# Kernel optimization log

Hardware: AMD Instinct MI355X
Metric: run time of the kernel (lower is better)

Reference implementation:

```python
import jax, jax.numpy as jnp
import numpy as np

EPS = 1e-8


def _mp_match(v1, v2, w):
    """Fused multi-perspective cosine match.
    v1, v2: (G, L, D); w: (P, D). Returns (G, L, P).
    cos_p(l) = <w_p*v1_l, w_p*v2_l> / max(||w_p*v1_l|| * ||w_p*v2_l||, eps)
    """
    w2 = w * w  # (P, D)
    num = jnp.einsum('gld,pd->glp', v1 * v2, w2)
    n1 = jnp.sqrt(jnp.einsum('gld,pd->glp', v1 * v1, w2))
    n2 = jnp.sqrt(jnp.einsum('gld,pd->glp', v2 * v2, w2))
    return num / jnp.maximum(n1 * n2, EPS)


def setup_inputs() -> dict:
    key = jax.random.key(0)
    k1, k2 = jax.random.split(key)
    n_graphs = 64
    nodes_per_graph = 2048
    dim = 128  # must equal perspectives (mp_w is square)
    N = n_graphs * nodes_per_graph
    feats = jax.random.normal(k1, (N, dim), dtype=jnp.float32)
    graph_idx = jnp.repeat(jnp.arange(n_graphs, dtype=jnp.int64), nodes_per_graph)
    mp_w = jax.random.uniform(k2, (dim, dim), dtype=jnp.float32)  # torch.rand
    return {"feats": feats, "mp_w": mp_w, "graph_idx": graph_idx, "n_graphs": n_graphs}


def reference(feats, mp_w, graph_idx, n_graphs):
    N, d = feats.shape
    L = N // n_graphs  # equal-size graphs, graph_idx is sorted/contiguous
    g = feats.reshape(n_graphs, L, d)
    p = g[0::2]  # (G/2, L, d) premise graphs
    h = g[1::2]  # (G/2, L, d) hypothesis graphs
    # cosine_attention is a plain dot product (no normalization in source)
    att = jnp.einsum('gld,gmd->glm', p, h)        # (G/2, Lp, Lh)
    att_p = jnp.einsum('glm,gmd->gld', att, h)     # (G/2, Lp, d)
    att_h = jnp.einsum('glm,gld->gmd', att, p)     # (G/2, Lh, d)
    multi_p = _mp_match(p, att_p, mp_w)            # (G/2, Lp, P)
    multi_h = _mp_match(h, att_h, mp_w)            # (G/2, Lh, P)
    # original concatenates [p0, h0, p1, h1, ...] along node axis
    P = mp_w.shape[0]
    out = jnp.stack([multi_p, multi_h], axis=1).reshape(n_graphs * L, P)
    return out
```

## Files before the change

kernel.cpp:

```cpp
#include <hip/hip_runtime.h>
#include <math.h>

#define D 128
#define GRAPHS 64

typedef __attribute__((ext_vector_type(8))) short bf16x8;
typedef __attribute__((ext_vector_type(4))) float f32x4;

union U4H8 { uint4 u; bf16x8 h; };

__device__ __forceinline__ unsigned short f2bf(float f) {
  union { float f; unsigned u; } v; v.f = f;
  unsigned r = v.u + 0x7fffu + ((v.u >> 16) & 1u);
  return (unsigned short)(r >> 16);
}
__device__ __forceinline__ unsigned asu(float f) {
  union { float f; unsigned u; } v; v.f = f; return v.u;
}
__device__ __forceinline__ float asf(unsigned u) {
  union { unsigned u; float f; } v; v.u = u; return v.f;
}

__device__ __forceinline__ int swzA(int u) {
  return u ^ (((((u >> 8) ^ (u >> 4)) & 3) ^ ((u >> 3) & 1)) << 1);
}
__device__ __forceinline__ int swzB(int u) {
  return u ^ ((((u >> 9) ^ (u >> 4)) & 3) << 1);
}

__global__ __launch_bounds__(256, 2) void gram_partial_kernel(
    const float* __restrict__ feats, unsigned short* __restrict__ partial,
    int L, int KS) {
  const int g = blockIdx.x / KS;
  const int sl = blockIdx.x - g * KS;
  const int chunk = L / KS;
  const float* __restrict__ X = feats + ((size_t)g * L + (size_t)sl * chunk) * D;

  __shared__ __align__(16) unsigned short smem[16384];
  const int tid = threadIdx.x;
  const int wv = tid >> 6, lane = tid & 63, quad = lane >> 4, ln = lane & 15;

  f32x4 acc[2][8];
#pragma unroll
  for (int rt = 0; rt < 2; ++rt)
#pragma unroll
    for (int ct = 0; ct < 8; ++ct) acc[rt][ct] = (f32x4)(0.f);

  int k2v[4], d4v[4];
#pragma unroll
  for (int v = 0; v < 4; ++v) {
    int tt = tid + v * 256;
    k2v[v] = tt & 31;
    d4v[v] = tt >> 5;
  }
  float4 pf[8];
#pragma unroll
  for (int v = 0; v < 4; ++v) {
    pf[2 * v] = *(const float4*)(X + (size_t)(2 * k2v[v]) * D + 4 * d4v[v]);
    pf[2 * v + 1] = *(const float4*)(X + (size_t)(2 * k2v[v] + 1) * D + 4 * d4v[v]);
  }

  for (int it = 0; it < chunk; it += 64) {
    __syncthreads();
#pragma unroll
    for (int v = 0; v < 4; ++v) {
      const float* p0 = (const float*)&pf[2 * v];
      const float* p1 = (const float*)&pf[2 * v + 1];
      int k = 2 * k2v[v];
      int ks = k >> 5, kk = k & 31, qs = kk >> 3, j = kk & 7;
#pragma unroll
      for (int i = 0; i < 4; ++i) {
        int d = 4 * d4v[v] + i, t = d >> 4, lnw = d & 15;
        *(unsigned*)&smem[((ks * 8 + t) * 64 + qs * 16 + lnw) * 8 + j] =
            (unsigned)f2bf(p0[i]) | ((unsigned)f2bf(p1[i]) << 16);
      }
    }
    __syncthreads();
    if (it + 64 < chunk) {
      const float* Xn = X + (size_t)(it + 64) * D;
#pragma unroll
      for (int v = 0; v < 4; ++v) {
        pf[2 * v] = *(const float4*)(Xn + (size_t)(2 * k2v[v]) * D + 4 * d4v[v]);
        pf[2 * v + 1] =
            *(const float4*)(Xn + (size_t)(2 * k2v[v] + 1) * D + 4 * d4v[v]);
      }
    }
#pragma unroll
    for (int ks = 0; ks < 2; ++ks) {
      bf16x8 af[2], bfr[8];
      af[0] = *(const bf16x8*)&smem[((ks * 8 + 2 * wv) * 64 + lane) * 8];
      af[1] = *(const bf16x8*)&smem[((ks * 8 + 2 * wv + 1) * 64 + lane) * 8];
#pragma unroll
      for (int ct = 0; ct < 8; ++ct)
        bfr[ct] = *(const bf16x8*)&smem[((ks * 8 + ct) * 64 + lane) * 8];
#pragma unroll
      for (int rt = 0; rt < 2; ++rt)
#pragma unroll
        for (int ct = 0; ct < 8; ++ct)
          acc[rt][ct] = __builtin_amdgcn_mfma_f32_16x16x32_bf16(
              af[rt], bfr[ct], acc[rt][ct], 0, 0, 0);
    }
  }

  __syncthreads();
#pragma unroll
  for (int rt = 0; rt < 2; ++rt)
#pragma unroll
    for (int ct = 0; ct < 8; ++ct)
#pragma unroll
      for (int r = 0; r < 4; ++r)
        smem[(32 * wv + 16 * rt + quad * 4 + r) * 128 + 16 * ct + ln] =
            f2bf(acc[rt][ct][r]);
  __syncthreads();
  unsigned short* P = partial + ((size_t)sl * GRAPHS + g) * (D * D);
#pragma unroll
  for (int v = 0; v < 8; ++v) {
    int idx = tid + v * 256;
    *(uint4*)&P[(size_t)idx * 8] = *(uint4*)&smem[idx * 8];
  }
}

__global__ __launch_bounds__(256) void reduce_w2_kernel(
    const unsigned short* __restrict__ partial, unsigned short* __restrict__ gram,
    const float* __restrict__ w, unsigned short* __restrict__ w2, int KS) {
  const int bid = blockIdx.x;
  if (bid < 512) {
    int idx = bid * 256 + threadIdx.x;
    int e8 = idx * 8;
    int g = e8 >> 14, e = e8 & (D * D - 1);
    float s[8];
#pragma unroll
    for (int i = 0; i < 8; ++i) s[i] = 0.f;
    for (int sl = 0; sl < KS; ++sl) {
      uint4 t = *(const uint4*)&partial[((size_t)sl * GRAPHS + g) * (D * D) + e];
      const unsigned* tp = &t.x;
#pragma unroll
      for (int q = 0; q < 4; ++q) {
        s[2 * q] += asf(tp[q] << 16);
        s[2 * q + 1] += asf(tp[q] & 0xFFFF0000u);
      }
    }
    uint4 o;
    o.x = (unsigned)f2bf(s[0]) | ((unsigned)f2bf(s[1]) << 16);
    o.y = (unsigned)f2bf(s[2]) | ((unsigned)f2bf(s[3]) << 16);
    o.z = (unsigned)f2bf(s[4]) | ((unsigned)f2bf(s[5]) << 16);
    o.w = (unsigned)f2bf(s[6]) | ((unsigned)f2bf(s[7]) << 16);
    *(uint4*)&gram[(size_t)g * (D * D) + e] = o;
  } else {
    int idx = (bid - 512) * 256 + threadIdx.x;
    const float* src = w + (size_t)idx * 8;
    float4 a = *(const float4*)src;
    float4 b = *(const float4*)(src + 4);
    uint4 o;
    o.x = (unsigned)f2bf(a.x * a.x) | ((unsigned)f2bf(a.y * a.y) << 16);
    o.y = (unsigned)f2bf(a.z * a.z) | ((unsigned)f2bf(a.w * a.w) << 16);
    o.z = (unsigned)f2bf(b.x * b.x) | ((unsigned)f2bf(b.y * b.y) << 16);
    o.w = (unsigned)f2bf(b.z * b.z) | ((unsigned)f2bf(b.w * b.w) << 16);
    *(uint4*)&w2[(size_t)idx * 8] = o;
  }
}

__global__ __launch_bounds__(512, 4) void fused_kernel4(
    const float* __restrict__ feats, const unsigned short* __restrict__ gram,
    const unsigned short* __restrict__ w2, float* __restrict__ out, int L) {
  const int tiles = L >> 6;
  const int gi = blockIdx.x / tiles;
  const int row0 = (blockIdx.x - gi * tiles) << 6;
  const float* __restrict__ A = feats + ((size_t)gi * L + row0) * D;
  const unsigned short* __restrict__ G = gram + (size_t)(gi ^ 1) * (D * D);
  float* __restrict__ O = out + ((size_t)gi * L + row0) * D;

  __shared__ __align__(16) unsigned short sAf[8192];
  __shared__ __align__(16) unsigned short sVf[8192];
  __shared__ __align__(16) unsigned short sBf[16384];

  const int tid = threadIdx.x;
  const int wv = tid >> 6, lane = tid & 63, quad = lane >> 4, ln = lane & 15;
  const int rowg = wv >> 1, colg = wv & 1;

#pragma unroll
  for (int v = 0; v < 4; ++v) {
    int idx = tid + v * 512;
    int r = idx >> 5, c4 = idx & 31;
    float4 t = *(const float4*)(A + (size_t)r * D + c4 * 4);
    int kc = c4 >> 3, qd = (c4 & 7) >> 1, j0 = (c4 & 1) * 4;
    int rt = r >> 4, lnw = r & 15;
    uint2 pk;
    pk.x = (unsigned)f2bf(t.x) | ((unsigned)f2bf(t.y) << 16);
    pk.y = (unsigned)f2bf(t.z) | ((unsigned)f2bf(t.w) << 16);
    *(uint2*)&sAf[swzA((kc * 4 + rt) * 64 + qd * 16 + lnw) * 8 + j0] = pk;
  }
#pragma unroll
  for (int v = 0; v < 4; ++v) {
    int idx = tid + v * 512;
    int r = idx >> 4, c16 = idx & 15;
    uint4 t = *(const uint4*)(G + (size_t)r * D + c16 * 8);
    int kc = c16 >> 2, qd = c16 & 3, tb = r >> 4, lnw = r & 15;
    *(uint4*)&sBf[swzB((kc * 8 + tb) * 64 + qd * 16 + lnw) * 8] = t;
  }
  __syncthreads();

  f32x4 acc1[4];
#pragma unroll
  for (int c = 0; c < 4; ++c) acc1[c] = (f32x4)(0.f);
#pragma unroll
  for (int kc = 0; kc < 4; ++kc) {
    bf16x8 af = *(const bf16x8*)&sAf[swzA((kc * 4 + rowg) * 64 + lane) * 8];
#pragma unroll
    for (int c = 0; c < 4; ++c) {
      int ct = colg * 4 + c;
      bf16x8 bfr = *(const bf16x8*)&sBf[swzB((kc * 8 + ct) * 64 + lane) * 8];
      acc1[c] = __builtin_amdgcn_mfma_f32_16x16x32_bf16(af, bfr, acc1[c], 0, 0, 0);
    }
  }
#pragma unroll
  for (int c = 0; c < 4; ++c)
#pragma unroll
    for (int r = 0; r < 4; ++r) {
      int col = (colg * 4 + c) * 16 + ln;
      int kc_t = col >> 5, q_t = (col >> 3) & 3, j_t = col & 7;
      sVf[swzA((kc_t * 4 + rowg) * 64 + q_t * 16 + quad * 4 + r) * 8 + j_t] =
          f2bf(acc1[c][r]);
    }
  __syncthreads();

#pragma unroll
  for (int v = 0; v < 4; ++v) {
    int idx = tid + v * 512;
    int r = idx >> 4, c16 = idx & 15;
    uint4 t = *(const uint4*)(w2 + (size_t)r * D + c16 * 8);
    int kc = c16 >> 2, qd = c16 & 3, tb = r >> 4, lnw = r & 15;
    *(uint4*)&sBf[swzB((kc * 8 + tb) * 64 + qd * 16 + lnw) * 8] = t;
  }
  __syncthreads();

  f32x4 an[4], s1[4], s2[4];
#pragma unroll
  for (int c = 0; c < 4; ++c) {
    an[c] = (f32x4)(0.f);
    s1[c] = (f32x4)(0.f);
    s2[c] = (f32x4)(0.f);
  }
#pragma unroll
  for (int dc = 0; dc < 4; ++dc) {
    uint4 ua = *(const uint4*)&sAf[swzA((dc * 4 + rowg) * 64 + lane) * 8];
    uint4 uv = *(const uint4*)&sVf[swzA((dc * 4 + rowg) * 64 + lane) * 8];
    U4H8 fx2, faa, fvv;
    const unsigned* uap = &ua.x;
    const unsigned* uvp = &uv.x;
#pragma unroll
    for (int q = 0; q < 4; ++q) {
      float a0 = asf(uap[q] << 16), a1 = asf(uap[q] & 0xFFFF0000u);
      float v0 = asf(uvp[q] << 16), v1 = asf(uvp[q] & 0xFFFF0000u);
      (&fx2.u.x)[q] = __builtin_amdgcn_perm(asu(a1 * v1), asu(a0 * v0), 0x07060302u);
      (&faa.u.x)[q] = __builtin_amdgcn_perm(asu(a1 * a1), asu(a0 * a0), 0x07060302u);
      (&fvv.u.x)[q] = __builtin_amdgcn_perm(asu(v1 * v1), asu(v0 * v0), 0x07060302u);
    }
#pragma unroll
    for (int c = 0; c < 4; ++c) {
      int ct = colg * 4 + c;
      bf16x8 wf = *(const bf16x8*)&sBf[swzB((dc * 8 + ct) * 64 + lane) * 8];
      an[c] = __builtin_amdgcn_mfma_f32_16x16x32_bf16(fx2.h, wf, an[c], 0, 0, 0);
      s1[c] = __builtin_amdgcn_mfma_f32_16x16x32_bf16(faa.h, wf, s1[c], 0, 0, 0);
      s2[c] = __builtin_amdgcn_mfma_f32_16x16x32_bf16(fvv.h, wf, s2[c], 0, 0, 0);
    }
  }

#pragma unroll
  for (int c = 0; c < 4; ++c)
#pragma unroll
    for (int r = 0; r < 4; ++r) {
      float t = fmaxf(s1[c][r] * s2[c][r], 1e-16f);
      O[(size_t)(rowg * 16 + quad * 4 + r) * D + (colg * 4 + c) * 16 + ln] =
          an[c][r] * __builtin_amdgcn_rsqf(t);
    }
}

extern "C" void kernel_launch(void* const* d_in, const int* in_sizes, int n_in,
                              void* d_out, int out_size, void* d_ws, size_t ws_size,
                              hipStream_t stream) {
  const float* feats = (const float*)d_in[0];
  const float* w = (const float*)d_in[1];
  float* out = (float*)d_out;
  const int L = (in_sizes[0] / D) / GRAPHS;

  const size_t partSlice = (size_t)GRAPHS * D * D * sizeof(unsigned short);
  const size_t gramB = partSlice;
  const size_t w2B = (size_t)D * D * sizeof(unsigned short);
  int KS = 16;
  while (KS > 1 && (size_t)KS * partSlice + gramB + w2B > ws_size) KS >>= 1;

  unsigned short* partialBuf = (unsigned short*)d_ws;
  unsigned short* gramBuf = partialBuf + (size_t)KS * GRAPHS * D * D;
  unsigned short* w2Buf = gramBuf + (size_t)GRAPHS * D * D;

  hipLaunchKernelGGL(gram_partial_kernel, dim3(GRAPHS * KS), dim3(256), 0,
                     stream, feats, partialBuf, L, KS);
  hipLaunchKernelGGL(reduce_w2_kernel, dim3(520), dim3(256), 0, stream,
                     partialBuf, gramBuf, w, w2Buf, KS);
  hipLaunchKernelGGL(fused_kernel4, dim3(GRAPHS * (L >> 6)), dim3(512), 0,
                     stream, feats, gramBuf, w2Buf, out, L);
}
```

Measured before the change: 157.0 us.

## Reuse A tile smem for attention output and split epilogue to raise occupancy

Drops the separate sVf shared buffer. The attention-weighted tile is written back into the sAf buffer after a barrier, and the original A fragments are kept in registers. The final multi-perspective MFMA stage is split into two passes over column pairs to cut accumulator register pressure, and launch bounds are raised to 6 blocks per CU. The goal is higher occupancy for this latency-bound fused kernel, at the cost of extra register-held fragments and recomputing the elementwise products per pass.

```diff
diff --git a/kernel.cpp b/kernel.cpp
--- a/kernel.cpp
+++ b/kernel.cpp
@@ -160,7 +160,7 @@
   }
 }
 
-__global__ __launch_bounds__(512, 4) void fused_kernel4(
+__global__ __launch_bounds__(512, 6) void fused_kernel4(
     const float* __restrict__ feats, const unsigned short* __restrict__ gram,
     const unsigned short* __restrict__ w2, float* __restrict__ out, int L) {
   const int tiles = L >> 6;
@@ -171,7 +171,6 @@
   float* __restrict__ O = out + ((size_t)gi * L + row0) * D;
 
   __shared__ __align__(16) unsigned short sAf[8192];
-  __shared__ __align__(16) unsigned short sVf[8192];
   __shared__ __align__(16) unsigned short sBf[16384];
 
   const int tid = threadIdx.x;
@@ -200,30 +199,32 @@
   }
   __syncthreads();
 
+  U4H8 uaf[4];
   f32x4 acc1[4];
 #pragma unroll
   for (int c = 0; c < 4; ++c) acc1[c] = (f32x4)(0.f);
 #pragma unroll
   for (int kc = 0; kc < 4; ++kc) {
-    bf16x8 af = *(const bf16x8*)&sAf[swzA((kc * 4 + rowg) * 64 + lane) * 8];
+    uaf[kc].u = *(const uint4*)&sAf[swzA((kc * 4 + rowg) * 64 + lane) * 8];
 #pragma unroll
     for (int c = 0; c < 4; ++c) {
       int ct = colg * 4 + c;
       bf16x8 bfr = *(const bf16x8*)&sBf[swzB((kc * 8 + ct) * 64 + lane) * 8];
-      acc1[c] = __builtin_amdgcn_mfma_f32_16x16x32_bf16(af, bfr, acc1[c], 0, 0, 0);
-    }
-  }
+      acc1[c] = __builtin_amdgcn_mfma_f32_16x16x32_bf16(uaf[kc].h, bfr,
+                                                        acc1[c], 0, 0, 0);
+    }
+  }
+  __syncthreads();
+
 #pragma unroll
   for (int c = 0; c < 4; ++c)
 #pragma unroll
     for (int r = 0; r < 4; ++r) {
       int col = (colg * 4 + c) * 16 + ln;
       int kc_t = col >> 5, q_t = (col >> 3) & 3, j_t = col & 7;
-      sVf[swzA((kc_t * 4 + rowg) * 64 + q_t * 16 + quad * 4 + r) * 8 + j_t] =
+      sAf[swzA((kc_t * 4 + rowg) * 64 + q_t * 16 + quad * 4 + r) * 8 + j_t] =
           f2bf(acc1[c][r]);
     }
-  __syncthreads();
-
 #pragma unroll
   for (int v = 0; v < 4; ++v) {
     int idx = tid + v * 512;
@@ -234,46 +235,52 @@
   }
   __syncthreads();
 
-  f32x4 an[4], s1[4], s2[4];
-#pragma unroll
-  for (int c = 0; c < 4; ++c) {
-    an[c] = (f32x4)(0.f);
-    s1[c] = (f32x4)(0.f);
-    s2[c] = (f32x4)(0.f);
-  }
-#pragma unroll
-  for (int dc = 0; dc < 4; ++dc) {
-    uint4 ua = *(const uint4*)&sAf[swzA((dc * 4 + rowg) * 64 + lane) * 8];
-    uint4 uv = *(const uint4*)&sVf[swzA((dc * 4 + rowg) * 64 + lane) * 8];
-    U4H8 fx2, faa, fvv;
-    const unsigned* uap = &ua.x;
-    const unsigned* uvp = &uv.x;
-#pragma unroll
-    for (int q = 0; q < 4; ++q) {
-      float a0 = asf(uap[q] << 16), a1 = asf(uap[q] & 0xFFFF0000u);
-      float v0 = asf(uvp[q] << 16), v1 = asf(uvp[q] & 0xFFFF0000u);
-      (&fx2.u.x)[q] = __builtin_amdgcn_perm(asu(a1 * v1), asu(a0 * v0), 0x07060302u);
-      (&faa.u.x)[q] = __builtin_amdgcn_perm(asu(a1 * a1), asu(a0 * a0), 0x07060302u);
-      (&fvv.u.x)[q] = __builtin_amdgcn_perm(asu(v1 * v1), asu(v0 * v0), 0x07060302u);
-    }
-#pragma unroll
-    for (int c = 0; c < 4; ++c) {
-      int ct = colg * 4 + c;
-      bf16x8 wf = *(const bf16x8*)&sBf[swzB((dc * 8 + ct) * 64 + lane) * 8];
-      an[c] = __builtin_amdgcn_mfma_f32_16x16x32_bf16(fx2.h, wf, an[c], 0, 0, 0);
-      s1[c] = __builtin_amdgcn_mfma_f32_16x16x32_bf16(faa.h, wf, s1[c], 0, 0, 0);
-      s2[c] = __builtin_amdgcn_mfma_f32_16x16x32_bf16(fvv.h, wf, s2[c], 0, 0, 0);
-    }
-  }
-
-#pragma unroll
-  for (int c = 0; c < 4; ++c)
-#pragma unroll
-    for (int r = 0; r < 4; ++r) {
-      float t = fmaxf(s1[c][r] * s2[c][r], 1e-16f);
-      O[(size_t)(rowg * 16 + quad * 4 + r) * D + (colg * 4 + c) * 16 + ln] =
-          an[c][r] * __builtin_amdgcn_rsqf(t);
-    }
+#pragma unroll
+  for (int cp = 0; cp < 2; ++cp) {
+    f32x4 an[2], s1[2], s2[2];
+#pragma unroll
+    for (int c = 0; c < 2; ++c) {
+      an[c] = (f32x4)(0.f);
+      s1[c] = (f32x4)(0.f);
+      s2[c] = (f32x4)(0.f);
+    }
+#pragma unroll
+    for (int dc = 0; dc < 4; ++dc) {
+      uint4 ua = uaf[dc].u;
+      uint4 uv = *(const uint4*)&sAf[swzA((dc * 4 + rowg) * 64 + lane) * 8];
+      U4H8 fx2, faa, fvv;
+      const unsigned* uap = &ua.x;
+      const unsigned* uvp = &uv.x;
+#pragma unroll
+      for (int q = 0; q < 4; ++q) {
+        float a0 = asf(uap[q] << 16), a1 = asf(uap[q] & 0xFFFF0000u);
+        float v0 = asf(uvp[q] << 16), v1 = asf(uvp[q] & 0xFFFF0000u);
+        (&fx2.u.x)[q] =
+            __builtin_amdgcn_perm(asu(a1 * v1), asu(a0 * v0), 0x07060302u);
+        (&faa.u.x)[q] =
+            __builtin_amdgcn_perm(asu(a1 * a1), asu(a0 * a0), 0x07060302u);
+        (&fvv.u.x)[q] =
+            __builtin_amdgcn_perm(asu(v1 * v1), asu(v0 * v0), 0x07060302u);
+      }
+#pragma unroll
+      for (int c = 0; c < 2; ++c) {
+        int ct = colg * 4 + cp * 2 + c;
+        bf16x8 wf = *(const bf16x8*)&sBf[swzB((dc * 8 + ct) * 64 + lane) * 8];
+        an[c] = __builtin_amdgcn_mfma_f32_16x16x32_bf16(fx2.h, wf, an[c], 0, 0, 0);
+        s1[c] = __builtin_amdgcn_mfma_f32_16x16x32_bf16(faa.h, wf, s1[c], 0, 0, 0);
+        s2[c] = __builtin_amdgcn_mfma_f32_16x16x32_bf16(fvv.h, wf, s2[c], 0, 0, 0);
+      }
+    }
+#pragma unroll
+    for (int c = 0; c < 2; ++c)
+#pragma unroll
+      for (int r = 0; r < 4; ++r) {
+        float t = fmaxf(s1[c][r] * s2[c][r], 1e-16f);
+        O[(size_t)(rowg * 16 + quad * 4 + r) * D +
+          (colg * 4 + cp * 2 + c) * 16 + ln] =
+            an[c][r] * __builtin_amdgcn_rsqf(t);
+      }
+  }
 }
 
 extern "C" void kernel_launch(void* const* d_in, const int* in_sizes, int n_in,
```

Result: slower. 267.0 us (+70.1%).

## Fuse split-K Gram reduction into partial kernel via last-block atomic counter

Applied to the files above, without the earlier changes.

Removes the separate reduce/w2 kernel. Each graph's last-finishing split-K block, found with a threadfence plus an atomic counter, sums the bf16 partials into the Gram matrix, and block 0 computes w squared. This saves a kernel launch and its dependency gap. In exchange it adds a memset launch for the counters, and the per-graph reduction now runs on only 64 blocks, serialized at the tail of the partial kernel.

```diff
diff --git a/kernel.cpp b/kernel.cpp
--- a/kernel.cpp
+++ b/kernel.cpp
@@ -30,15 +30,34 @@
 
 __global__ __launch_bounds__(256, 2) void gram_partial_kernel(
     const float* __restrict__ feats, unsigned short* __restrict__ partial,
-    int L, int KS) {
+    unsigned short* __restrict__ gram, const float* __restrict__ w,
+    unsigned short* __restrict__ w2, int* __restrict__ counters, int L,
+    int KS) {
   const int g = blockIdx.x / KS;
   const int sl = blockIdx.x - g * KS;
   const int chunk = L / KS;
   const float* __restrict__ X = feats + ((size_t)g * L + (size_t)sl * chunk) * D;
 
   __shared__ __align__(16) unsigned short smem[16384];
+  __shared__ int sLast;
   const int tid = threadIdx.x;
   const int wv = tid >> 6, lane = tid & 63, quad = lane >> 4, ln = lane & 15;
+
+  if (blockIdx.x == 0) {
+#pragma unroll
+    for (int grp = 0; grp < 8; ++grp) {
+      int idx = tid + grp * 256;
+      const float* src = w + (size_t)idx * 8;
+      float4 a = *(const float4*)src;
+      float4 b = *(const float4*)(src + 4);
+      uint4 o;
+      o.x = (unsigned)f2bf(a.x * a.x) | ((unsigned)f2bf(a.y * a.y) << 16);
+      o.y = (unsigned)f2bf(a.z * a.z) | ((unsigned)f2bf(a.w * a.w) << 16);
+      o.z = (unsigned)f2bf(b.x * b.x) | ((unsigned)f2bf(b.y * b.y) << 16);
+      o.w = (unsigned)f2bf(b.z * b.z) | ((unsigned)f2bf(b.w * b.w) << 16);
+      *(uint4*)&w2[(size_t)idx * 8] = o;
+    }
+  }
 
   f32x4 acc[2][8];
 #pragma unroll
@@ -118,45 +137,40 @@
     int idx = tid + v * 256;
     *(uint4*)&P[(size_t)idx * 8] = *(uint4*)&smem[idx * 8];
   }
-}
-
-__global__ __launch_bounds__(256) void reduce_w2_kernel(
-    const unsigned short* __restrict__ partial, unsigned short* __restrict__ gram,
-    const float* __restrict__ w, unsigned short* __restrict__ w2, int KS) {
-  const int bid = blockIdx.x;
-  if (bid < 512) {
-    int idx = bid * 256 + threadIdx.x;
-    int e8 = idx * 8;
-    int g = e8 >> 14, e = e8 & (D * D - 1);
-    float s[8];
-#pragma unroll
-    for (int i = 0; i < 8; ++i) s[i] = 0.f;
-    for (int sl = 0; sl < KS; ++sl) {
-      uint4 t = *(const uint4*)&partial[((size_t)sl * GRAPHS + g) * (D * D) + e];
-      const unsigned* tp = &t.x;
-#pragma unroll
-      for (int q = 0; q < 4; ++q) {
-        s[2 * q] += asf(tp[q] << 16);
-        s[2 * q + 1] += asf(tp[q] & 0xFFFF0000u);
+
+  __threadfence();
+  __syncthreads();
+  if (tid == 0) {
+    int old = atomicAdd(&counters[g], 1);
+    sLast = (old == KS - 1) ? 1 : 0;
+  }
+  __syncthreads();
+  if (sLast) {
+    __threadfence();
+    const int DD = D * D;
+#pragma unroll
+    for (int grp = 0; grp < 8; ++grp) {
+      int idx = tid + grp * 256;
+      int e = idx * 8;
+      float s[8];
+#pragma unroll
+      for (int i = 0; i < 8; ++i) s[i] = 0.f;
+      for (int s2 = 0; s2 < KS; ++s2) {
+        uint4 t = *(const uint4*)&partial[((size_t)s2 * GRAPHS + g) * DD + e];
+        const unsigned* tp = &t.x;
+#pragma unroll
+        for (int q = 0; q < 4; ++q) {
+          s[2 * q] += asf(tp[q] << 16);
+          s[2 * q + 1] += asf(tp[q] & 0xFFFF0000u);
+        }
       }
-    }
-    uint4 o;
-    o.x = (unsigned)f2bf(s[0]) | ((unsigned)f2bf(s[1]) << 16);
-    o.y = (unsigned)f2bf(s[2]) | ((unsigned)f2bf(s[3]) << 16);
-    o.z = (unsigned)f2bf(s[4]) | ((unsigned)f2bf(s[5]) << 16);
-    o.w = (unsigned)f2bf(s[6]) | ((unsigned)f2bf(s[7]) << 16);
-    *(uint4*)&gram[(size_t)g * (D * D) + e] = o;
-  } else {
-    int idx = (bid - 512) * 256 + threadIdx.x;
-    const float* src = w + (size_t)idx * 8;
-    float4 a = *(const float4*)src;
-    float4 b = *(const float4*)(src + 4);
-    uint4 o;
-    o.x = (unsigned)f2bf(a.x * a.x) | ((unsigned)f2bf(a.y * a.y) << 16);
-    o.y = (unsigned)f2bf(a.z * a.z) | ((unsigned)f2bf(a.w * a.w) << 16);
-    o.z = (unsigned)f2bf(b.x * b.x) | ((unsigned)f2bf(b.y * b.y) << 16);
-    o.w = (unsigned)f2bf(b.z * b.z) | ((unsigned)f2bf(b.w * b.w) << 16);
-    *(uint4*)&w2[(size_t)idx * 8] = o;
+      uint4 o;
+      o.x = (unsigned)f2bf(s[0]) | ((unsigned)f2bf(s[1]) << 16);
+      o.y = (unsigned)f2bf(s[2]) | ((unsigned)f2bf(s[3]) << 16);
+      o.z = (unsigned)f2bf(s[4]) | ((unsigned)f2bf(s[5]) << 16);
+      o.w = (unsigned)f2bf(s[6]) | ((unsigned)f2bf(s[7]) << 16);
+      *(uint4*)&gram[(size_t)g * DD + e] = o;
+    }
   }
 }
 
@@ -287,17 +301,19 @@
   const size_t partSlice = (size_t)GRAPHS * D * D * sizeof(unsigned short);
   const size_t gramB = partSlice;
   const size_t w2B = (size_t)D * D * sizeof(unsigned short);
+  const size_t cntB = (size_t)GRAPHS * sizeof(int);
   int KS = 16;
-  while (KS > 1 && (size_t)KS * partSlice + gramB + w2B > ws_size) KS >>= 1;
+  while (KS > 1 && (size_t)KS * partSlice + gramB + w2B + cntB > ws_size) KS >>= 1;
 
   unsigned short* partialBuf = (unsigned short*)d_ws;
   unsigned short* gramBuf = partialBuf + (size_t)KS * GRAPHS * D * D;
   unsigned short* w2Buf = gramBuf + (size_t)GRAPHS * D * D;
-
+  int* countersBuf = (int*)(w2Buf + (size_t)D * D);
+
+  hipMemsetAsync(countersBuf, 0, cntB, stream);
   hipLaunchKernelGGL(gram_partial_kernel, dim3(GRAPHS * KS), dim3(256), 0,
-                     stream, feats, partialBuf, L, KS);
-  hipLaunchKernelGGL(reduce_w2_kernel, dim3(520), dim3(256), 0, stream,
-                     partialBuf, gramBuf, w, w2Buf, KS);
+                     stream, feats, partialBuf, gramBuf, w, w2Buf, countersBuf,
+                     L, KS);
   hipLaunchKernelGGL(fused_kernel4, dim3(GRAPHS * (L >> 6)), dim3(512), 0,
                      stream, feats, gramBuf, w2Buf, out, L);
 }
```

New measurement: 364.4 us. +132.2%, slower.
